# Performance work log

Measured on AMD Instinct MI355X. Metric: run time of the kernel, lower is better.

## Reference

```python
import jax, jax.numpy as jnp
import numpy as np

B, N, D = 16, 1024, 768
H = 12
HS = D // H
L = 2  # n_ffn_layers
EPS = 1e-6


def layernorm(x, scale, bias):
    mu = jnp.mean(x, axis=-1, keepdims=True)
    var = jnp.var(x, axis=-1, keepdims=True)
    return (x - mu) * jax.lax.rsqrt(var + EPS) * scale + bias


def log_cosh(x):
    # numerically stable log(cosh(x)) = |x| + log1p(exp(-2|x|)) - log(2)
    ax = jnp.abs(x)
    return ax + jnp.log1p(jnp.exp(-2.0 * ax)) - jnp.log(2.0)


def setup_inputs() -> dict:
    key = jax.random.key(0)
    ks = jax.random.split(key, 8)
    x = jax.random.normal(ks[0], (B, N, D), dtype=jnp.float32)
    # pre-attention LayerNorm params
    ln1_scale = jnp.ones((D,), jnp.float32)
    ln1_bias = jnp.zeros((D,), jnp.float32)
    # per-head value projections [H, D, HS] (Dense, no bias)
    Wv = jax.random.normal(ks[1], (H, D, HS), jnp.float32) / np.sqrt(D)
    # per-head circulant rows alpha_delta [H, N], truncated_normal(stddev=sqrt(1/N))
    alpha = jax.random.truncated_normal(ks[2], -2.0, 2.0, (H, N), jnp.float32) * np.sqrt(1.0 / N)
    # FFN: L layers of Dense(D) + LayerNorm + swish
    Wf = jax.random.normal(ks[3], (L, D, D), jnp.float32) / np.sqrt(D)
    bf = jnp.zeros((L, D), jnp.float32)
    lnf_scale = jnp.ones((L, D), jnp.float32)
    lnf_bias = jnp.zeros((L, D), jnp.float32)
    return {"x": x, "ln1_scale": ln1_scale, "ln1_bias": ln1_bias, "Wv": Wv,
            "alpha": alpha, "Wf": Wf, "bf": bf,
            "lnf_scale": lnf_scale, "lnf_bias": lnf_bias}


def reference(x, ln1_scale, ln1_bias, Wv, alpha, Wf, bf, lnf_scale, lnf_bias):
    b, n, d = x.shape
    h, hs = Wv.shape[0], Wv.shape[2]
    # --- multi-head positional (circulant) attention on LN(x) ---
    xn = layernorm(x, ln1_scale, ln1_bias)
    v = jnp.einsum('bnd,hdk->bhnk', xn, Wv)  # per-head values
    # circulant matrix C[h, i, j] = alpha[h, (i - j) mod n]  (scipy.linalg.circulant)
    idx = (jnp.arange(n)[:, None] - jnp.arange(n)[None, :]) % n  # [n, n]
    C = alpha[:, idx]                                            # [h, n, n]
    y = jnp.einsum('hij,bhjk->bhik', C, v)                       # [b, h, n, hs]
    y = jnp.transpose(y, (0, 2, 1, 3)).reshape(b, n, h * hs)     # concat heads
    x = x + y
    # --- FFN: [Dense(D) -> LayerNorm -> swish] x L ---
    z = x
    for l in range(Wf.shape[0]):
        z = jax.nn.swish(layernorm(z @ Wf[l] + bf[l], lnf_scale[l], lnf_bias[l]))
    return log_cosh(z + x)
```

## Files before the change

kernel.cpp:

```cpp
#include <hip/hip_runtime.h>
#include <cstdint>
#include <cstddef>


typedef __attribute__((ext_vector_type(8))) short bf16x8;
typedef __attribute__((ext_vector_type(4))) float f32x4;
typedef __attribute__((ext_vector_type(4))) unsigned short us4;

__device__ __forceinline__ unsigned short f2bf(float f) {
  unsigned int u = __builtin_bit_cast(unsigned int, f);
  u += 0x7FFFu + ((u >> 16) & 1u);
  return (unsigned short)(u >> 16);
}

__device__ __forceinline__ void g2l16(const void* g, void* l) {
  __builtin_amdgcn_global_load_lds(
      (const __attribute__((address_space(1))) unsigned int*)g,
      (__attribute__((address_space(3))) unsigned int*)l,
      16, 0, 0);
}

__global__ __launch_bounds__(256) void pack_w2t(const float* __restrict__ Wv,
                                                unsigned short* __restrict__ W2t) {
  int o = blockIdx.x * 256 + threadIdx.x;
  int np = o / 768, d = o - np * 768;
  int h = np >> 6, k = np & 63;
  W2t[o] = f2bf(Wv[h * 49152 + d * 64 + k]);
}

__global__ __launch_bounds__(256) void pack_wft(const float* __restrict__ Wf,
                                                unsigned short* __restrict__ Wft) {
  int o = blockIdx.x * 256 + threadIdx.x;
  int l = o / 589824, rem = o - l * 589824;
  int np = rem / 768, d = rem - np * 768;
  Wft[o] = f2bf(Wf[l * 589824 + d * 768 + np]);
}

__global__ __launch_bounds__(256) void pack_c(const float* __restrict__ alpha,
                                              unsigned short* __restrict__ Cbf) {
  int o = blockIdx.x * 256 + threadIdx.x;
  int h = o >> 20, i = (o >> 10) & 1023, j = o & 1023;
  Cbf[o] = f2bf(alpha[(h << 10) + ((i - j) & 1023)]);
}

__device__ __forceinline__ void wave_reduce2(float& s, float& s2) {
#pragma unroll
  for (int off = 32; off > 0; off >>= 1) {
    s += __shfl_down(s, off);
    s2 += __shfl_down(s2, off);
  }
  s = __shfl(s, 0);
  s2 = __shfl(s2, 0);
}

__global__ __launch_bounds__(256) void ln1_kernel(const float* __restrict__ x,
                                                  const float* __restrict__ sc,
                                                  const float* __restrict__ bi,
                                                  unsigned short* __restrict__ out) {
  int row = blockIdx.x * 4 + (threadIdx.x >> 6);
  int lane = threadIdx.x & 63;
  size_t base = (size_t)row * 768;
  float4 v[3];
#pragma unroll
  for (int j = 0; j < 3; ++j) v[j] = *(const float4*)(x + base + lane * 4 + j * 256);
  float s = 0.f, s2 = 0.f;
#pragma unroll
  for (int j = 0; j < 3; ++j) {
    s += v[j].x + v[j].y + v[j].z + v[j].w;
    s2 += v[j].x * v[j].x + v[j].y * v[j].y + v[j].z * v[j].z + v[j].w * v[j].w;
  }
  wave_reduce2(s, s2);
  float mu = s * (1.0f / 768.0f);
  float var = s2 * (1.0f / 768.0f) - mu * mu;
  float r = rsqrtf(var + 1e-6f);
#pragma unroll
  for (int j = 0; j < 3; ++j) {
    int d = lane * 4 + j * 256;
    float4 scv = *(const float4*)(sc + d);
    float4 biv = *(const float4*)(bi + d);
    us4 o;
    o[0] = f2bf((v[j].x - mu) * r * scv.x + biv.x);
    o[1] = f2bf((v[j].y - mu) * r * scv.y + biv.y);
    o[2] = f2bf((v[j].z - mu) * r * scv.z + biv.z);
    o[3] = f2bf((v[j].w - mu) * r * scv.w + biv.w);
    *(us4*)(out + base + d) = o;
  }
}

__global__ __launch_bounds__(256) void lnswish_kernel(const float* __restrict__ g,
                                                      const float* __restrict__ sc,
                                                      const float* __restrict__ bi,
                                                      unsigned short* __restrict__ out) {
  int row = blockIdx.x * 4 + (threadIdx.x >> 6);
  int lane = threadIdx.x & 63;
  size_t base = (size_t)row * 768;
  float4 v[3];
#pragma unroll
  for (int j = 0; j < 3; ++j) v[j] = *(const float4*)(g + base + lane * 4 + j * 256);
  float s = 0.f, s2 = 0.f;
#pragma unroll
  for (int j = 0; j < 3; ++j) {
    s += v[j].x + v[j].y + v[j].z + v[j].w;
    s2 += v[j].x * v[j].x + v[j].y * v[j].y + v[j].z * v[j].z + v[j].w * v[j].w;
  }
  wave_reduce2(s, s2);
  float mu = s * (1.0f / 768.0f);
  float var = s2 * (1.0f / 768.0f) - mu * mu;
  float r = rsqrtf(var + 1e-6f);
#pragma unroll
  for (int j = 0; j < 3; ++j) {
    int d = lane * 4 + j * 256;
    float4 scv = *(const float4*)(sc + d);
    float4 biv = *(const float4*)(bi + d);
    float zz[4] = {(v[j].x - mu) * r * scv.x + biv.x, (v[j].y - mu) * r * scv.y + biv.y,
                   (v[j].z - mu) * r * scv.z + biv.z, (v[j].w - mu) * r * scv.w + biv.w};
    us4 o;
#pragma unroll
    for (int q = 0; q < 4; ++q) o[q] = f2bf(zz[q] / (1.0f + __expf(-zz[q])));
    *(us4*)(out + base + d) = o;
  }
}

__global__ __launch_bounds__(256) void final_kernel(const float* __restrict__ g,
                                                    const float* __restrict__ sc,
                                                    const float* __restrict__ bi,
                                                    float* __restrict__ out) {
  int row = blockIdx.x * 4 + (threadIdx.x >> 6);
  int lane = threadIdx.x & 63;
  size_t base = (size_t)row * 768;
  float4 v[3];
#pragma unroll
  for (int j = 0; j < 3; ++j) v[j] = *(const float4*)(g + base + lane * 4 + j * 256);
  float s = 0.f, s2 = 0.f;
#pragma unroll
  for (int j = 0; j < 3; ++j) {
    s += v[j].x + v[j].y + v[j].z + v[j].w;
    s2 += v[j].x * v[j].x + v[j].y * v[j].y + v[j].z * v[j].z + v[j].w * v[j].w;
  }
  wave_reduce2(s, s2);
  float mu = s * (1.0f / 768.0f);
  float var = s2 * (1.0f / 768.0f) - mu * mu;
  float r = rsqrtf(var + 1e-6f);
#pragma unroll
  for (int j = 0; j < 3; ++j) {
    int d = lane * 4 + j * 256;
    float4 scv = *(const float4*)(sc + d);
    float4 biv = *(const float4*)(bi + d);
    float4 xv = *(const float4*)(out + base + d);
    float zz[4] = {(v[j].x - mu) * r * scv.x + biv.x, (v[j].y - mu) * r * scv.y + biv.y,
                   (v[j].z - mu) * r * scv.z + biv.z, (v[j].w - mu) * r * scv.w + biv.w};
    float xx[4] = {xv.x, xv.y, xv.z, xv.w};
    float4 o;
    float* op = &o.x;
#pragma unroll
    for (int q = 0; q < 4; ++q) {
      float sw = zz[q] / (1.0f + __expf(-zz[q]));
      float t = sw + xx[q];
      float ax = fabsf(t);
      op[q] = ax + __logf(1.0f + __expf(-2.0f * ax)) - 0.69314718055994531f;
    }
    *(float4*)(out + base + d) = o;
  }
}

__device__ __forceinline__ void gemm_core(const unsigned short* __restrict__ A,
                                          const unsigned short* __restrict__ Bt,
                                          int K, int m0, int n0,
                                          unsigned short* sA, unsigned short* sB,
                                          f32x4 acc[4][4]) {
  const int tid = threadIdx.x;
  const int wave = tid >> 6, lane = tid & 63;
  const int wm = (wave >> 1) << 6, wn = (wave & 1) << 6;
  const int fm = lane & 15, fq = lane >> 4;
  const int r0 = tid >> 2, r1 = (tid >> 2) + 64;
  const int cg = tid & 3;
  const int cs0 = (cg ^ ((r0 >> 1) & 3)) << 3;
  const int cs1 = (cg ^ ((r1 >> 1) & 3)) << 3;
  const int ld0 = r0 * 32 + (cg << 3);
  const int ld1 = r1 * 32 + (cg << 3);

  const int niter = K >> 5;
#define STAGE(k0, buf)                                                        \
  {                                                                           \
    unsigned short* dA = sA + (buf) * 4096;                                   \
    unsigned short* dB = sB + (buf) * 4096;                                   \
    g2l16(A + (size_t)(m0 + r0) * K + (k0) + cs0, dA + ld0);                  \
    g2l16(Bt + (size_t)(n0 + r0) * K + (k0) + cs0, dB + ld0);                 \
    g2l16(A + (size_t)(m0 + r1) * K + (k0) + cs1, dA + ld1);                  \
    g2l16(Bt + (size_t)(n0 + r1) * K + (k0) + cs1, dB + ld1);                 \
  }

  STAGE(0, 0);
  for (int it = 0; it < niter; ++it) {
    int buf = it & 1;
    __syncthreads();
    if (it + 1 < niter) STAGE((it + 1) << 5, buf ^ 1);
    const unsigned short* pA = sA + buf * 4096;
    const unsigned short* pB = sB + buf * 4096;
    bf16x8 aq[4], bq[4];
#pragma unroll
    for (int t = 0; t < 4; ++t) {
      int ra = wm + (t << 4) + fm;
      int rb = wn + (t << 4) + fm;
      aq[t] = *(const bf16x8*)(pA + (ra << 5) + ((fq ^ ((ra >> 1) & 3)) << 3));
      bq[t] = *(const bf16x8*)(pB + (rb << 5) + ((fq ^ ((rb >> 1) & 3)) << 3));
    }
#pragma unroll
    for (int mt = 0; mt < 4; ++mt)
#pragma unroll
      for (int nt = 0; nt < 4; ++nt)
        acc[mt][nt] = __builtin_amdgcn_mfma_f32_16x16x32_bf16(aq[mt], bq[nt],
                                                              acc[mt][nt], 0, 0, 0);
  }
#undef STAGE
}

__device__ __forceinline__ void decode_mn_768(int f, int& m0, int& n0) {
  int xcd = f & 7, s = f >> 3;
  int g = s / 6, bx = s - g * 6;
  m0 = (xcd + g * 8) << 7;
  n0 = bx << 7;
}

__global__ __launch_bounds__(256, 4) void gemm1_kernel(const unsigned short* __restrict__ A,
                                                       const unsigned short* __restrict__ Bt,
                                                       unsigned short* __restrict__ Vt) {
  __shared__ unsigned short sA[2 * 128 * 32];
  __shared__ unsigned short sB[2 * 128 * 32];
  f32x4 acc[4][4] = {};
  int m0, n0;
  decode_mn_768(blockIdx.x, m0, n0);
  gemm_core(A, Bt, 768, m0, n0, sA, sB, acc);
  const int wave = threadIdx.x >> 6, lane = threadIdx.x & 63;
  const int wm = (wave >> 1) << 6, wn = (wave & 1) << 6;
  const int fm = lane & 15, fq = lane >> 4;
#pragma unroll
  for (int mt = 0; mt < 4; ++mt) {
    int rowb = m0 + wm + (mt << 4) + (fq << 2);
    int b = rowb >> 10, n = rowb & 1023;
#pragma unroll
    for (int nt = 0; nt < 4; ++nt) {
      int col = n0 + wn + (nt << 4) + fm;
      int h = col >> 6, ck = col & 63;
      size_t off = ((size_t)h << 20) + (size_t)((b << 6) + ck) * 1024 + n;
      us4 v;
#pragma unroll
      for (int r = 0; r < 4; ++r) v[r] = f2bf(acc[mt][nt][r]);
      *(us4*)(Vt + off) = v;
    }
  }
}

__global__ __launch_bounds__(256, 4) void circ_kernel(const unsigned short* __restrict__ Cbf,
                                                      const unsigned short* __restrict__ Vt,
                                                      const float* __restrict__ xin,
                                                      float* __restrict__ x2f,
                                                      unsigned short* __restrict__ x2bf) {
  __shared__ unsigned short sA[2 * 128 * 32];
  __shared__ unsigned short sB[2 * 128 * 32];
  f32x4 acc[4][4] = {};
  int f = blockIdx.x;
  int xcd = f & 7, s = f >> 3;
  int h = s >> 3, t = s & 7;
  int mr = xcd >> 1, nr = xcd & 1;
  int m0 = ((mr << 1) + (t >> 2)) << 7;
  int n0 = ((nr << 2) + (t & 3)) << 7;
  gemm_core(Cbf + ((size_t)h << 20), Vt + ((size_t)h << 20), 1024, m0, n0, sA, sB, acc);
  const int wave = threadIdx.x >> 6, lane = threadIdx.x & 63;
  const int wm = (wave >> 1) << 6, wn = (wave & 1) << 6;
  const int fm = lane & 15, fq = lane >> 4;
#pragma unroll
  for (int mt = 0; mt < 4; ++mt) {
    int ib = m0 + wm + (mt << 4) + (fq << 2);
#pragma unroll
    for (int nt = 0; nt < 4; ++nt) {
      int c = n0 + wn + (nt << 4) + fm;
      int b = c >> 6, k = c & 63;
      size_t off = ((size_t)(b << 10) + ib) * 768 + (h << 6) + k;
#pragma unroll
      for (int r = 0; r < 4; ++r) {
        float val = acc[mt][nt][r] + xin[off + (size_t)r * 768];
        x2f[off + (size_t)r * 768] = val;
        x2bf[off + (size_t)r * 768] = f2bf(val);
      }
    }
  }
}

__global__ __launch_bounds__(256, 4) void gemmf_kernel(const unsigned short* __restrict__ A,
                                                       const unsigned short* __restrict__ Bt,
                                                       const float* __restrict__ bias,
                                                       float* __restrict__ g) {
  __shared__ unsigned short sA[2 * 128 * 32];
  __shared__ unsigned short sB[2 * 128 * 32];
  f32x4 acc[4][4] = {};
  int m0, n0;
  decode_mn_768(blockIdx.x, m0, n0);
  gemm_core(A, Bt, 768, m0, n0, sA, sB, acc);
  const int wave = threadIdx.x >> 6, lane = threadIdx.x & 63;
  const int wm = (wave >> 1) << 6, wn = (wave & 1) << 6;
  const int fm = lane & 15, fq = lane >> 4;
#pragma unroll
  for (int mt = 0; mt < 4; ++mt) {
    int rowb = m0 + wm + (mt << 4) + (fq << 2);
#pragma unroll
    for (int nt = 0; nt < 4; ++nt) {
      int col = n0 + wn + (nt << 4) + fm;
      float bc = bias[col];
#pragma unroll
      for (int r = 0; r < 4; ++r)
        g[(size_t)(rowb + r) * 768 + col] = acc[mt][nt][r] + bc;
    }
  }
}

extern "C" void kernel_launch(void* const* d_in, const int* in_sizes, int n_in,
                              void* d_out, int out_size, void* d_ws, size_t ws_size,
                              hipStream_t stream) {
  const float* x = (const float*)d_in[0];
  const float* ln1_s = (const float*)d_in[1];
  const float* ln1_b = (const float*)d_in[2];
  const float* Wv = (const float*)d_in[3];
  const float* alpha = (const float*)d_in[4];
  const float* Wf = (const float*)d_in[5];
  const float* bf = (const float*)d_in[6];
  const float* lnf_s = (const float*)d_in[7];
  const float* lnf_b = (const float*)d_in[8];
  float* out = (float*)d_out;

  char* ws = (char*)d_ws;
  unsigned short* slotA = (unsigned short*)ws;
  unsigned short* Vt = (unsigned short*)(ws + 25165824);
  unsigned short* Cbf = (unsigned short*)(ws + 50331648);
  float* g = (float*)(ws + 25165824);
  unsigned short* W2t = (unsigned short*)(ws + 75497472);
  unsigned short* Wft = (unsigned short*)(ws + 76677120);

  pack_w2t<<<2304, 256, 0, stream>>>(Wv, W2t);
  pack_wft<<<4608, 256, 0, stream>>>(Wf, Wft);
  pack_c<<<49152, 256, 0, stream>>>(alpha, Cbf);

  ln1_kernel<<<4096, 256, 0, stream>>>(x, ln1_s, ln1_b, slotA);
  gemm1_kernel<<<768, 256, 0, stream>>>(slotA, W2t, Vt);
  circ_kernel<<<768, 256, 0, stream>>>(Cbf, Vt, x, out, slotA);
  gemmf_kernel<<<768, 256, 0, stream>>>(slotA, Wft, bf, g);
  lnswish_kernel<<<4096, 256, 0, stream>>>(g, lnf_s, lnf_b, slotA);
  gemmf_kernel<<<768, 256, 0, stream>>>(slotA, Wft + 589824, bf + 768, g);
  final_kernel<<<4096, 256, 0, stream>>>(g, lnf_s + 768, lnf_b + 768, out);
}
```

Measured before the change: 316.1 us.

## Build circulant tiles in LDS, deepen GEMM pipeline, store intermediates as bf16

The pack_c kernel, which materialized a 24MB bf16 circulant matrix, is removed. circ_kernel now fills a small LDS buffer directly from alpha in eight shifted copies, which keeps the vector loads aligned, and streams only V through a 4-stage async pipeline. gemm_core moves from double to triple buffering with explicit vmcnt waits, lowering occupancy bounds to 3. The GEMM outputs g and the residual x2 are now kept only as bf16 instead of fp32, cutting memory traffic at some cost in precision for the final residual and layernorm inputs.

```diff
diff --git a/kernel.cpp b/kernel.cpp
--- a/kernel.cpp
+++ b/kernel.cpp
@@ -11,6 +11,9 @@
   unsigned int u = __builtin_bit_cast(unsigned int, f);
   u += 0x7FFFu + ((u >> 16) & 1u);
   return (unsigned short)(u >> 16);
+}
+__device__ __forceinline__ float bf2f(unsigned short u) {
+  return __builtin_bit_cast(float, (unsigned int)u << 16);
 }
 
 __device__ __forceinline__ void g2l16(const void* g, void* l) {
@@ -19,6 +22,8 @@
       (__attribute__((address_space(3))) unsigned int*)l,
       16, 0, 0);
 }
+
+#define WAITB(n) asm volatile("s_waitcnt vmcnt(" #n ") lgkmcnt(0)\n\ts_barrier" ::: "memory")
 
 __global__ __launch_bounds__(256) void pack_w2t(const float* __restrict__ Wv,
                                                 unsigned short* __restrict__ W2t) {
@@ -34,13 +39,6 @@
   int l = o / 589824, rem = o - l * 589824;
   int np = rem / 768, d = rem - np * 768;
   Wft[o] = f2bf(Wf[l * 589824 + d * 768 + np]);
-}
-
-__global__ __launch_bounds__(256) void pack_c(const float* __restrict__ alpha,
-                                              unsigned short* __restrict__ Cbf) {
-  int o = blockIdx.x * 256 + threadIdx.x;
-  int h = o >> 20, i = (o >> 10) & 1023, j = o & 1023;
-  Cbf[o] = f2bf(alpha[(h << 10) + ((i - j) & 1023)]);
 }
 
 __device__ __forceinline__ void wave_reduce2(float& s, float& s2) {
@@ -87,22 +85,25 @@
   }
 }
 
-__global__ __launch_bounds__(256) void lnswish_kernel(const float* __restrict__ g,
+__global__ __launch_bounds__(256) void lnswish_kernel(const unsigned short* __restrict__ g,
                                                       const float* __restrict__ sc,
                                                       const float* __restrict__ bi,
                                                       unsigned short* __restrict__ out) {
   int row = blockIdx.x * 4 + (threadIdx.x >> 6);
   int lane = threadIdx.x & 63;
   size_t base = (size_t)row * 768;
-  float4 v[3];
-#pragma unroll
-  for (int j = 0; j < 3; ++j) v[j] = *(const float4*)(g + base + lane * 4 + j * 256);
+  float v[3][4];
+#pragma unroll
+  for (int j = 0; j < 3; ++j) {
+    us4 gv = *(const us4*)(g + base + lane * 4 + j * 256);
+#pragma unroll
+    for (int q = 0; q < 4; ++q) v[j][q] = bf2f(gv[q]);
+  }
   float s = 0.f, s2 = 0.f;
 #pragma unroll
-  for (int j = 0; j < 3; ++j) {
-    s += v[j].x + v[j].y + v[j].z + v[j].w;
-    s2 += v[j].x * v[j].x + v[j].y * v[j].y + v[j].z * v[j].z + v[j].w * v[j].w;
-  }
+  for (int j = 0; j < 3; ++j)
+#pragma unroll
+    for (int q = 0; q < 4; ++q) { s += v[j][q]; s2 += v[j][q] * v[j][q]; }
   wave_reduce2(s, s2);
   float mu = s * (1.0f / 768.0f);
   float var = s2 * (1.0f / 768.0f) - mu * mu;
@@ -112,31 +113,38 @@
     int d = lane * 4 + j * 256;
     float4 scv = *(const float4*)(sc + d);
     float4 biv = *(const float4*)(bi + d);
-    float zz[4] = {(v[j].x - mu) * r * scv.x + biv.x, (v[j].y - mu) * r * scv.y + biv.y,
-                   (v[j].z - mu) * r * scv.z + biv.z, (v[j].w - mu) * r * scv.w + biv.w};
+    const float* scp = &scv.x;
+    const float* bip = &biv.x;
     us4 o;
 #pragma unroll
-    for (int q = 0; q < 4; ++q) o[q] = f2bf(zz[q] / (1.0f + __expf(-zz[q])));
+    for (int q = 0; q < 4; ++q) {
+      float z = (v[j][q] - mu) * r * scp[q] + bip[q];
+      o[q] = f2bf(z / (1.0f + __expf(-z)));
+    }
     *(us4*)(out + base + d) = o;
   }
 }
 
-__global__ __launch_bounds__(256) void final_kernel(const float* __restrict__ g,
+__global__ __launch_bounds__(256) void final_kernel(const unsigned short* __restrict__ g,
                                                     const float* __restrict__ sc,
                                                     const float* __restrict__ bi,
+                                                    const unsigned short* __restrict__ x2,
                                                     float* __restrict__ out) {
   int row = blockIdx.x * 4 + (threadIdx.x >> 6);
   int lane = threadIdx.x & 63;
   size_t base = (size_t)row * 768;
-  float4 v[3];
-#pragma unroll
-  for (int j = 0; j < 3; ++j) v[j] = *(const float4*)(g + base + lane * 4 + j * 256);
+  float v[3][4];
+#pragma unroll
+  for (int j = 0; j < 3; ++j) {
+    us4 gv = *(const us4*)(g + base + lane * 4 + j * 256);
+#pragma unroll
+    for (int q = 0; q < 4; ++q) v[j][q] = bf2f(gv[q]);
+  }
   float s = 0.f, s2 = 0.f;
 #pragma unroll
-  for (int j = 0; j < 3; ++j) {
-    s += v[j].x + v[j].y + v[j].z + v[j].w;
-    s2 += v[j].x * v[j].x + v[j].y * v[j].y + v[j].z * v[j].z + v[j].w * v[j].w;
-  }
+  for (int j = 0; j < 3; ++j)
+#pragma unroll
+    for (int q = 0; q < 4; ++q) { s += v[j][q]; s2 += v[j][q] * v[j][q]; }
   wave_reduce2(s, s2);
   float mu = s * (1.0f / 768.0f);
   float var = s2 * (1.0f / 768.0f) - mu * mu;
@@ -146,16 +154,16 @@
     int d = lane * 4 + j * 256;
     float4 scv = *(const float4*)(sc + d);
     float4 biv = *(const float4*)(bi + d);
-    float4 xv = *(const float4*)(out + base + d);
-    float zz[4] = {(v[j].x - mu) * r * scv.x + biv.x, (v[j].y - mu) * r * scv.y + biv.y,
-                   (v[j].z - mu) * r * scv.z + biv.z, (v[j].w - mu) * r * scv.w + biv.w};
-    float xx[4] = {xv.x, xv.y, xv.z, xv.w};
+    us4 xv = *(const us4*)(x2 + base + d);
+    const float* scp = &scv.x;
+    const float* bip = &biv.x;
     float4 o;
     float* op = &o.x;
 #pragma unroll
     for (int q = 0; q < 4; ++q) {
-      float sw = zz[q] / (1.0f + __expf(-zz[q]));
-      float t = sw + xx[q];
+      float z = (v[j][q] - mu) * r * scp[q] + bip[q];
+      float sw = z / (1.0f + __expf(-z));
+      float t = sw + bf2f(xv[q]);
       float ax = fabsf(t);
       op[q] = ax + __logf(1.0f + __expf(-2.0f * ax)) - 0.69314718055994531f;
     }
@@ -172,46 +180,54 @@
   const int wave = tid >> 6, lane = tid & 63;
   const int wm = (wave >> 1) << 6, wn = (wave & 1) << 6;
   const int fm = lane & 15, fq = lane >> 4;
-  const int r0 = tid >> 2, r1 = (tid >> 2) + 64;
+  const int r0 = tid >> 2, r1 = r0 + 64;
   const int cg = tid & 3;
   const int cs0 = (cg ^ ((r0 >> 1) & 3)) << 3;
   const int cs1 = (cg ^ ((r1 >> 1) & 3)) << 3;
   const int ld0 = r0 * 32 + (cg << 3);
   const int ld1 = r1 * 32 + (cg << 3);
-
   const int niter = K >> 5;
-#define STAGE(k0, buf)                                                        \
+
+#define STAGE(k0v, buf)                                                       \
   {                                                                           \
     unsigned short* dA = sA + (buf) * 4096;                                   \
     unsigned short* dB = sB + (buf) * 4096;                                   \
-    g2l16(A + (size_t)(m0 + r0) * K + (k0) + cs0, dA + ld0);                  \
-    g2l16(Bt + (size_t)(n0 + r0) * K + (k0) + cs0, dB + ld0);                 \
-    g2l16(A + (size_t)(m0 + r1) * K + (k0) + cs1, dA + ld1);                  \
-    g2l16(Bt + (size_t)(n0 + r1) * K + (k0) + cs1, dB + ld1);                 \
+    g2l16(A + (size_t)(m0 + r0) * K + (k0v) + cs0, dA + ld0);                 \
+    g2l16(Bt + (size_t)(n0 + r0) * K + (k0v) + cs0, dB + ld0);                \
+    g2l16(A + (size_t)(m0 + r1) * K + (k0v) + cs1, dA + ld1);                 \
+    g2l16(Bt + (size_t)(n0 + r1) * K + (k0v) + cs1, dB + ld1);                \
+  }
+#define GCOMP(bc)                                                             \
+  {                                                                           \
+    const unsigned short* pA = sA + (bc) * 4096;                              \
+    const unsigned short* pB = sB + (bc) * 4096;                              \
+    bf16x8 aq[4], bq[4];                                                      \
+    _Pragma("unroll") for (int t = 0; t < 4; ++t) {                           \
+      int ra = wm + (t << 4) + fm;                                            \
+      int rb = wn + (t << 4) + fm;                                            \
+      aq[t] = *(const bf16x8*)(pA + (ra << 5) + ((fq ^ ((ra >> 1) & 3)) << 3)); \
+      bq[t] = *(const bf16x8*)(pB + (rb << 5) + ((fq ^ ((rb >> 1) & 3)) << 3)); \
+    }                                                                         \
+    _Pragma("unroll") for (int mt = 0; mt < 4; ++mt)                          \
+    _Pragma("unroll") for (int nt = 0; nt < 4; ++nt)                          \
+      acc[mt][nt] = __builtin_amdgcn_mfma_f32_16x16x32_bf16(aq[mt], bq[nt],   \
+                                                            acc[mt][nt], 0, 0, 0); \
   }
 
   STAGE(0, 0);
-  for (int it = 0; it < niter; ++it) {
-    int buf = it & 1;
-    __syncthreads();
-    if (it + 1 < niter) STAGE((it + 1) << 5, buf ^ 1);
-    const unsigned short* pA = sA + buf * 4096;
-    const unsigned short* pB = sB + buf * 4096;
-    bf16x8 aq[4], bq[4];
-#pragma unroll
-    for (int t = 0; t < 4; ++t) {
-      int ra = wm + (t << 4) + fm;
-      int rb = wn + (t << 4) + fm;
-      aq[t] = *(const bf16x8*)(pA + (ra << 5) + ((fq ^ ((ra >> 1) & 3)) << 3));
-      bq[t] = *(const bf16x8*)(pB + (rb << 5) + ((fq ^ ((rb >> 1) & 3)) << 3));
-    }
-#pragma unroll
-    for (int mt = 0; mt < 4; ++mt)
-#pragma unroll
-      for (int nt = 0; nt < 4; ++nt)
-        acc[mt][nt] = __builtin_amdgcn_mfma_f32_16x16x32_bf16(aq[mt], bq[nt],
-                                                              acc[mt][nt], 0, 0, 0);
-  }
+  STAGE(32, 1);
+  int bs = 2, bc = 0;
+  for (int it = 0; it < niter - 1; ++it) {
+    WAITB(4);
+    if (it + 2 < niter) {
+      STAGE((it + 2) << 5, bs);
+      bs = (bs == 2) ? 0 : bs + 1;
+    }
+    GCOMP(bc);
+    bc = (bc == 2) ? 0 : bc + 1;
+  }
+  WAITB(0);
+  GCOMP(bc);
 #undef STAGE
 }
 
@@ -222,11 +238,11 @@
   n0 = bx << 7;
 }
 
-__global__ __launch_bounds__(256, 4) void gemm1_kernel(const unsigned short* __restrict__ A,
+__global__ __launch_bounds__(256, 3) void gemm1_kernel(const unsigned short* __restrict__ A,
                                                        const unsigned short* __restrict__ Bt,
                                                        unsigned short* __restrict__ Vt) {
-  __shared__ unsigned short sA[2 * 128 * 32];
-  __shared__ unsigned short sB[2 * 128 * 32];
+  __shared__ unsigned short sA[3 * 4096];
+  __shared__ unsigned short sB[3 * 4096];
   f32x4 acc[4][4] = {};
   int m0, n0;
   decode_mn_768(blockIdx.x, m0, n0);
@@ -251,13 +267,12 @@
   }
 }
 
-__global__ __launch_bounds__(256, 4) void circ_kernel(const unsigned short* __restrict__ Cbf,
+__global__ __launch_bounds__(256, 3) void circ_kernel(const float* __restrict__ alpha,
                                                       const unsigned short* __restrict__ Vt,
                                                       const float* __restrict__ xin,
-                                                      float* __restrict__ x2f,
                                                       unsigned short* __restrict__ x2bf) {
-  __shared__ unsigned short sA[2 * 128 * 32];
-  __shared__ unsigned short sB[2 * 128 * 32];
+  __shared__ unsigned short sAc[8 * 1168];
+  __shared__ unsigned short sB[4 * 4096];
   f32x4 acc[4][4] = {};
   int f = blockIdx.x;
   int xcd = f & 7, s = f >> 3;
@@ -265,10 +280,66 @@
   int mr = xcd >> 1, nr = xcd & 1;
   int m0 = ((mr << 1) + (t >> 2)) << 7;
   int n0 = ((nr << 2) + (t & 3)) << 7;
-  gemm_core(Cbf + ((size_t)h << 20), Vt + ((size_t)h << 20), 1024, m0, n0, sA, sB, acc);
-  const int wave = threadIdx.x >> 6, lane = threadIdx.x & 63;
+
+  const int tid = threadIdx.x;
+  const int wave = tid >> 6, lane = tid & 63;
   const int wm = (wave >> 1) << 6, wn = (wave & 1) << 6;
   const int fm = lane & 15, fq = lane >> 4;
+
+  const float* ah = alpha + (h << 10);
+#pragma unroll
+  for (int c = 0; c < 8; ++c)
+    for (int u = tid; u < 1160; u += 256)
+      sAc[c * 1168 + u] = f2bf(ah[(m0 - 897 - u - c) & 1023]);
+  asm volatile("s_waitcnt vmcnt(0)" ::: "memory");
+
+  const unsigned short* Bt = Vt + ((size_t)h << 20);
+  const int r0 = tid >> 2, r1 = r0 + 64;
+  const int cg = tid & 3;
+  const int cs0 = (cg ^ ((r0 >> 1) & 3)) << 3;
+  const int cs1 = (cg ^ ((r1 >> 1) & 3)) << 3;
+  const int ld0 = r0 * 32 + (cg << 3);
+  const int ld1 = r1 * 32 + (cg << 3);
+
+#define STAGEB(k0v, buf)                                                      \
+  {                                                                           \
+    unsigned short* dB = sB + (buf) * 4096;                                   \
+    g2l16(Bt + (size_t)(n0 + r0) * 1024 + (k0v) + cs0, dB + ld0);             \
+    g2l16(Bt + (size_t)(n0 + r1) * 1024 + (k0v) + cs1, dB + ld1);             \
+  }
+#define CCOMP(it)                                                             \
+  {                                                                           \
+    const unsigned short* pB = sB + ((it) & 3) * 4096;                        \
+    int k0v = (it) << 5;                                                      \
+    bf16x8 aq[4], bq[4];                                                      \
+    _Pragma("unroll") for (int t_ = 0; t_ < 4; ++t_) {                        \
+      int rl = wm + (t_ << 4) + fm;                                           \
+      int d = k0v + (fq << 3) + 127 - rl;                                     \
+      int c = d & 7;                                                          \
+      aq[t_] = *(const bf16x8*)(sAc + c * 1168 + (d - c));                    \
+      int rb = wn + (t_ << 4) + fm;                                           \
+      bq[t_] = *(const bf16x8*)(pB + (rb << 5) + ((fq ^ ((rb >> 1) & 3)) << 3)); \
+    }                                                                         \
+    _Pragma("unroll") for (int mt = 0; mt < 4; ++mt)                          \
+    _Pragma("unroll") for (int nt = 0; nt < 4; ++nt)                          \
+      acc[mt][nt] = __builtin_amdgcn_mfma_f32_16x16x32_bf16(aq[mt], bq[nt],   \
+                                                            acc[mt][nt], 0, 0, 0); \
+  }
+
+  STAGEB(0, 0);
+  STAGEB(32, 1);
+  STAGEB(64, 2);
+  for (int it = 0; it < 30; ++it) {
+    WAITB(4);
+    if (it < 29) STAGEB((it + 3) << 5, (it + 3) & 3);
+    CCOMP(it);
+  }
+  WAITB(2);
+  CCOMP(30);
+  WAITB(0);
+  CCOMP(31);
+#undef STAGEB
+
 #pragma unroll
   for (int mt = 0; mt < 4; ++mt) {
     int ib = m0 + wm + (mt << 4) + (fq << 2);
@@ -280,19 +351,18 @@
 #pragma unroll
       for (int r = 0; r < 4; ++r) {
         float val = acc[mt][nt][r] + xin[off + (size_t)r * 768];
-        x2f[off + (size_t)r * 768] = val;
         x2bf[off + (size_t)r * 768] = f2bf(val);
       }
     }
   }
 }
 
-__global__ __launch_bounds__(256, 4) void gemmf_kernel(const unsigned short* __restrict__ A,
+__global__ __launch_bounds__(256, 3) void gemmf_kernel(const unsigned short* __restrict__ A,
                                                        const unsigned short* __restrict__ Bt,
                                                        const float* __restrict__ bias,
-                                                       float* __restrict__ g) {
-  __shared__ unsigned short sA[2 * 128 * 32];
-  __shared__ unsigned short sB[2 * 128 * 32];
+                                                       unsigned short* __restrict__ g) {
+  __shared__ unsigned short sA[3 * 4096];
+  __shared__ unsigned short sB[3 * 4096];
   f32x4 acc[4][4] = {};
   int m0, n0;
   decode_mn_768(blockIdx.x, m0, n0);
@@ -309,7 +379,7 @@
       float bc = bias[col];
 #pragma unroll
       for (int r = 0; r < 4; ++r)
-        g[(size_t)(rowb + r) * 768 + col] = acc[mt][nt][r] + bc;
+        g[(size_t)(rowb + r) * 768 + col] = f2bf(acc[mt][nt][r] + bc);
     }
   }
 }
@@ -331,20 +401,19 @@
   char* ws = (char*)d_ws;
   unsigned short* slotA = (unsigned short*)ws;
   unsigned short* Vt = (unsigned short*)(ws + 25165824);
-  unsigned short* Cbf = (unsigned short*)(ws + 50331648);
-  float* g = (float*)(ws + 25165824);
+  unsigned short* gbf = Vt;
+  unsigned short* slotX = (unsigned short*)(ws + 50331648);
   unsigned short* W2t = (unsigned short*)(ws + 75497472);
   unsigned short* Wft = (unsigned short*)(ws + 76677120);
 
   pack_w2t<<<2304, 256, 0, stream>>>(Wv, W2t);
   pack_wft<<<4608, 256, 0, stream>>>(Wf, Wft);
-  pack_c<<<49152, 256, 0, stream>>>(alpha, Cbf);
 
   ln1_kernel<<<4096, 256, 0, stream>>>(x, ln1_s, ln1_b, slotA);
   gemm1_kernel<<<768, 256, 0, stream>>>(slotA, W2t, Vt);
-  circ_kernel<<<768, 256, 0, stream>>>(Cbf, Vt, x, out, slotA);
-  gemmf_kernel<<<768, 256, 0, stream>>>(slotA, Wft, bf, g);
-  lnswish_kernel<<<4096, 256, 0, stream>>>(g, lnf_s, lnf_b, slotA);
-  gemmf_kernel<<<768, 256, 0, stream>>>(slotA, Wft + 589824, bf + 768, g);
-  final_kernel<<<4096, 256, 0, stream>>>(g, lnf_s + 768, lnf_b + 768, out);
-}
+  circ_kernel<<<768, 256, 0, stream>>>(alpha, Vt, x, slotX);
+  gemmf_kernel<<<768, 256, 0, stream>>>(slotX, Wft, bf, gbf);
+  lnswish_kernel<<<4096, 256, 0, stream>>>(gbf, lnf_s, lnf_b, slotA);
+  gemmf_kernel<<<768, 256, 0, stream>>>(slotA, Wft + 589824, bf + 768, gbf);
+  final_kernel<<<4096, 256, 0, stream>>>(gbf, lnf_s + 768, lnf_b + 768, slotX, out);
+}
```

Result: faster. 278.0 us (-12.1%).
